# Kernel tuning notes

Hardware: AMD Instinct MI355X
Metric: run time of the kernel (lower is better)

Reference implementation:

```python
import jax, jax.numpy as jnp
import numpy as np

TOP_K = 8
N_GROUP = 8
TOPK_GROUP = 4
ROUTED_SCALING_FACTOR = 2.5
NUM_TOKENS = 131072
NUM_EXPERTS = 256


def setup_inputs() -> dict:
    key = jax.random.key(0)
    k1, k2 = jax.random.split(key)
    logits = jax.random.normal(k1, (NUM_TOKENS, NUM_EXPERTS), dtype=jnp.float32)
    e_score_correction_bias = jax.random.normal(k2, (NUM_EXPERTS,), dtype=jnp.float32)
    return {"logits": logits, "e_score_correction_bias": e_score_correction_bias}


def reference(logits, e_score_correction_bias):
    T, E = logits.shape
    eg = E // N_GROUP  # experts per group
    scores = jax.nn.sigmoid(logits)                       # [T, E]
    swb = scores + e_score_correction_bias                # [T, E]

    # group score = sum of top-2 biased scores within each group
    swb_g = swb.reshape(T, N_GROUP, eg)
    group_scores = jax.lax.top_k(swb_g, 2)[0].sum(-1)     # [T, G]

    # select topk_group groups, build group mask
    group_idx = jax.lax.top_k(group_scores, TOPK_GROUP)[1]  # [T, KG]
    rows = jnp.arange(T)[:, None]
    group_mask = jnp.zeros((T, N_GROUP), dtype=swb.dtype).at[rows, group_idx].set(1.0)
    score_mask = jnp.broadcast_to(group_mask[:, :, None], (T, N_GROUP, eg)).reshape(T, E)

    # mask out non-selected groups, top-k over biased scores
    neg_inf = jnp.array(-jnp.inf, dtype=swb.dtype)
    swb_masked = jnp.where(score_mask > 0, swb, neg_inf)
    topk_idx = jax.lax.top_k(swb_masked, TOP_K)[1]        # [T, K]

    # keep only selected experts' unbiased scores, renormalize, scale
    new_mask = jnp.zeros((T, E), dtype=scores.dtype).at[rows, topk_idx].set(1.0)
    s = scores * new_mask
    s = s / (s.sum(-1, keepdims=True) + 1e-20) * ROUTED_SCALING_FACTOR

    topk_values, topk_indices = jax.lax.top_k(s, TOP_K)   # [T, K]
    return topk_indices.astype(jnp.int32), topk_values.astype(jnp.float32)
```

## Files before the change

### kernel.cpp

```cpp
#include <hip/hip_runtime.h>
#include <cstdint>


constexpr int TOPK_GROUP  = 4;
constexpr int TOP_K       = 8;
constexpr float ROUTED_SCALING = 2.5f;
constexpr unsigned KEY_OFF = 0x3F000000u;

#define DPP_XOR1 0xB1
#define DPP_XOR2 0x4E
#define DPP_HM   0x141
#define DPP_M    0x140

template <int CTRL>
static __device__ __forceinline__ float dpp_f32(float x) {
  return __int_as_float(__builtin_amdgcn_mov_dpp(__float_as_int(x), CTRL, 0xF, 0xF, true));
}
template <int CTRL>
static __device__ __forceinline__ unsigned dpp_u32(unsigned x) {
  return (unsigned)__builtin_amdgcn_mov_dpp((int)x, CTRL, 0xF, 0xF, true);
}

static __device__ __forceinline__ int mbcnt64(unsigned long long m) {
  return __builtin_amdgcn_mbcnt_hi((unsigned)(m >> 32),
         __builtin_amdgcn_mbcnt_lo((unsigned)m, 0));
}

static __device__ __forceinline__ unsigned umax2(unsigned x, unsigned y) {
  return x > y ? x : y;
}

__global__ __launch_bounds__(256) void moe_route_kernel(
    const float* __restrict__ logits,
    const float* __restrict__ bias,
    float* __restrict__ out_idx,
    float* __restrict__ out_val,
    int n_tokens) {
  const int lane = threadIdx.x & 63;
  const int wid  = threadIdx.x >> 6;
  const int token = blockIdx.x * 4 + wid;
  __shared__ float2 buf[4][16];

  const float4 lv = reinterpret_cast<const float4*>(logits)[token * 64 + lane];
  const float4 bv = reinterpret_cast<const float4*>(bias)[lane];

  const float sig0 = __builtin_amdgcn_rcpf(1.0f + __builtin_amdgcn_exp2f(lv.x * -1.44269504f));
  const float sig1 = __builtin_amdgcn_rcpf(1.0f + __builtin_amdgcn_exp2f(lv.y * -1.44269504f));
  const float sig2 = __builtin_amdgcn_rcpf(1.0f + __builtin_amdgcn_exp2f(lv.z * -1.44269504f));
  const float sig3 = __builtin_amdgcn_rcpf(1.0f + __builtin_amdgcn_exp2f(lv.w * -1.44269504f));
  const float swb0 = sig0 + bv.x;
  const float swb1 = sig1 + bv.y;
  const float swb2 = sig2 + bv.z;
  const float swb3 = sig3 + bv.w;

  const float h1 = fmaxf(swb0, swb1), l1 = fminf(swb0, swb1);
  const float h2 = fmaxf(swb2, swb3), l2 = fminf(swb2, swb3);
  float m1 = fmaxf(h1, h2);
  float m2 = fmaxf(fminf(h1, h2), fmaxf(l1, l2));
#define MERGE_LEV(CTRL)                                            \
  {                                                                \
    const float o1 = dpp_f32<CTRL>(m1);                            \
    const float o2 = dpp_f32<CTRL>(m2);                            \
    const float nm1 = fmaxf(m1, o1);                               \
    const float nm2 = fmaxf(fminf(m1, o1), fmaxf(m2, o2));         \
    m1 = nm1; m2 = nm2;                                            \
  }
  MERGE_LEV(DPP_XOR1)
  MERGE_LEV(DPP_XOR2)
  MERGE_LEV(DPP_HM)
#undef MERGE_LEV
  const float gscore = m1 + m2;

  const int g = lane >> 3;
  const int a = lane & 7;
  const float gs_o = __shfl(gscore, a << 3);
  const unsigned long long gm =
      __ballot((gs_o > gscore) || (gs_o == gscore && a < g));
  const int grank = __popc((unsigned)(gm >> (g << 3)) & 0xFFu);
  const bool gsel = grank < TOPK_GROUP;

  const int ebase = lane << 2;
  const unsigned k0 = gsel ? ((unsigned)__float_as_int(fmaxf(swb0, 0.5f)) - KEY_OFF) : 0u;
  const unsigned k1 = gsel ? ((unsigned)__float_as_int(fmaxf(swb1, 0.5f)) - KEY_OFF) : 0u;
  const unsigned k2 = gsel ? ((unsigned)__float_as_int(fmaxf(swb2, 0.5f)) - KEY_OFF) : 0u;
  const unsigned k3 = gsel ? ((unsigned)__float_as_int(fmaxf(swb3, 0.5f)) - KEY_OFF) : 0u;

  unsigned tf = 0u;
  for (int bit = 24; bit >= 16; --bit) {
    const unsigned cand = tf | (1u << bit);
    const int c = __popcll(__ballot(k0 >= cand)) + __popcll(__ballot(k1 >= cand))
                + __popcll(__ballot(k2 >= cand)) + __popcll(__ballot(k3 >= cand));
    if (c >= TOP_K) {
      tf = cand;
      if (c == TOP_K) break;
    }
  }

  bool sel0 = k0 >= tf, sel1 = k1 >= tf, sel2 = k2 >= tf, sel3 = k3 >= tf;
  unsigned long long sm0 = __ballot(sel0), sm1 = __ballot(sel1),
                     sm2 = __ballot(sel2), sm3 = __ballot(sel3);
  const int cnt = __popcll(sm0) + __popcll(sm1) + __popcll(sm2) + __popcll(sm3);

  if (cnt > TOP_K) {
    const unsigned tg = tf + 0x10000u;
    const bool c0 = sel0 && (k0 < tg);
    const bool c1 = sel1 && (k1 < tg);
    const bool c2 = sel2 && (k2 < tg);
    const bool c3 = sel3 && (k3 < tg);
    const int nc = __popcll(__ballot(c0)) + __popcll(__ballot(c1))
                 + __popcll(__ballot(c2)) + __popcll(__ballot(c3));
    const int need2 = TOP_K - (cnt - nc);
    sel0 = sel0 && !c0; sel1 = sel1 && !c1;
    sel2 = sel2 && !c2; sel3 = sel3 && !c3;
    unsigned p0 = c0 ? (((k0 & 0xFFFFu) << 16) | (0xFFFFu - (unsigned)(ebase + 0))) : 0u;
    unsigned p1 = c1 ? (((k1 & 0xFFFFu) << 16) | (0xFFFFu - (unsigned)(ebase + 1))) : 0u;
    unsigned p2 = c2 ? (((k2 & 0xFFFFu) << 16) | (0xFFFFu - (unsigned)(ebase + 2))) : 0u;
    unsigned p3 = c3 ? (((k3 & 0xFFFFu) << 16) | (0xFFFFu - (unsigned)(ebase + 3))) : 0u;
    for (int r = 0; r < need2; ++r) {
      unsigned mm = umax2(umax2(p0, p1), umax2(p2, p3));
      mm = umax2(mm, dpp_u32<DPP_XOR1>(mm));
      mm = umax2(mm, dpp_u32<DPP_XOR2>(mm));
      mm = umax2(mm, dpp_u32<DPP_HM>(mm));
      mm = umax2(mm, dpp_u32<DPP_M>(mm));
      mm = umax2(mm, (unsigned)__shfl_xor((int)mm, 16));
      mm = umax2(mm, (unsigned)__shfl_xor((int)mm, 32));
      const bool w0 = (p0 == mm), w1 = (p1 == mm), w2 = (p2 == mm), w3 = (p3 == mm);
      sel0 = sel0 || w0; sel1 = sel1 || w1;
      sel2 = sel2 || w2; sel3 = sel3 || w3;
      p0 = w0 ? 0u : p0; p1 = w1 ? 0u : p1;
      p2 = w2 ? 0u : p2; p3 = w3 ? 0u : p3;
    }
    sm0 = __ballot(sel0); sm1 = __ballot(sel1);
    sm2 = __ballot(sel2); sm3 = __ballot(sel3);
  }

  const int sbelow = mbcnt64(sm0) + mbcnt64(sm1) + mbcnt64(sm2) + mbcnt64(sm3);
  const int slot0 = sbelow;
  const int slot1 = slot0 + (int)sel0;
  const int slot2 = slot1 + (int)sel1;
  const int slot3 = slot2 + (int)sel2;

  float2* tb = buf[wid];
  tb[sel0 ? slot0 : 8]  = make_float2(__int_as_float(ebase + 0), sig0);
  tb[sel1 ? slot1 : 9]  = make_float2(__int_as_float(ebase + 1), sig1);
  tb[sel2 ? slot2 : 10] = make_float2(__int_as_float(ebase + 2), sig2);
  tb[sel3 ? slot3 : 11] = make_float2(__int_as_float(ebase + 3), sig3);
  asm volatile("s_waitcnt lgkmcnt(0)" ::: "memory");

  const int l8 = lane & 7;
  const float2 w  = tb[l8];
  const float2 wo = tb[lane >> 3];
  const float wsig = w.y;
  float ssum = wsig;
  ssum += dpp_f32<DPP_XOR1>(ssum);
  ssum += dpp_f32<DPP_XOR2>(ssum);
  ssum += dpp_f32<DPP_HM>(ssum);
  const float inv = __builtin_amdgcn_rcpf(ssum);
  const float val = wsig * inv * ROUTED_SCALING;
  const float v_o = wo.y * inv * ROUTED_SCALING;
  const int widx_i = __float_as_int(w.x);
  const int i_o_i  = __float_as_int(wo.x);

  const unsigned long long rm =
      __ballot((val > v_o) || (val == v_o && widx_i < i_o_i));
  const int rank = __popc((unsigned)(rm >> (l8 << 3)) & 0xFFu);

  if (lane < 16) {
    float* base = (lane < 8) ? out_idx : out_val;
    base[token * TOP_K + rank] = (lane < 8) ? (float)widx_i : val;
  }
}

extern "C" void kernel_launch(void* const* d_in, const int* in_sizes, int n_in,
                              void* d_out, int out_size, void* d_ws, size_t ws_size,
                              hipStream_t stream) {
  const float* logits = (const float*)d_in[0];
  const float* bias   = (const float*)d_in[1];
  float* out = (float*)d_out;

  const int n_tokens = in_sizes[0] / 256;
  float* out_idx = out;
  float* out_val = out + (size_t)n_tokens * TOP_K;

  const int blocks = (n_tokens + 3) / 4;
  moe_route_kernel<<<blocks, 256, 0, stream>>>(logits, bias, out_idx, out_val, n_tokens);
}
```

Measured before the change: 41.05 us.

## Process two tokens per wavefront with interleaved selection for ILP

Result: slower. 44.44 us (+8.3%).

```diff
diff --git a/kernel.cpp b/kernel.cpp
--- a/kernel.cpp
+++ b/kernel.cpp
@@ -30,72 +30,15 @@
   return x > y ? x : y;
 }
 
-__global__ __launch_bounds__(256) void moe_route_kernel(
-    const float* __restrict__ logits,
-    const float* __restrict__ bias,
-    float* __restrict__ out_idx,
-    float* __restrict__ out_val,
-    int n_tokens) {
-  const int lane = threadIdx.x & 63;
-  const int wid  = threadIdx.x >> 6;
-  const int token = blockIdx.x * 4 + wid;
-  __shared__ float2 buf[4][16];
-
-  const float4 lv = reinterpret_cast<const float4*>(logits)[token * 64 + lane];
-  const float4 bv = reinterpret_cast<const float4*>(bias)[lane];
-
-  const float sig0 = __builtin_amdgcn_rcpf(1.0f + __builtin_amdgcn_exp2f(lv.x * -1.44269504f));
-  const float sig1 = __builtin_amdgcn_rcpf(1.0f + __builtin_amdgcn_exp2f(lv.y * -1.44269504f));
-  const float sig2 = __builtin_amdgcn_rcpf(1.0f + __builtin_amdgcn_exp2f(lv.z * -1.44269504f));
-  const float sig3 = __builtin_amdgcn_rcpf(1.0f + __builtin_amdgcn_exp2f(lv.w * -1.44269504f));
-  const float swb0 = sig0 + bv.x;
-  const float swb1 = sig1 + bv.y;
-  const float swb2 = sig2 + bv.z;
-  const float swb3 = sig3 + bv.w;
-
-  const float h1 = fmaxf(swb0, swb1), l1 = fminf(swb0, swb1);
-  const float h2 = fmaxf(swb2, swb3), l2 = fminf(swb2, swb3);
-  float m1 = fmaxf(h1, h2);
-  float m2 = fmaxf(fminf(h1, h2), fmaxf(l1, l2));
-#define MERGE_LEV(CTRL)                                            \
-  {                                                                \
-    const float o1 = dpp_f32<CTRL>(m1);                            \
-    const float o2 = dpp_f32<CTRL>(m2);                            \
-    const float nm1 = fmaxf(m1, o1);                               \
-    const float nm2 = fmaxf(fminf(m1, o1), fmaxf(m2, o2));         \
-    m1 = nm1; m2 = nm2;                                            \
-  }
-  MERGE_LEV(DPP_XOR1)
-  MERGE_LEV(DPP_XOR2)
-  MERGE_LEV(DPP_HM)
-#undef MERGE_LEV
-  const float gscore = m1 + m2;
-
-  const int g = lane >> 3;
-  const int a = lane & 7;
-  const float gs_o = __shfl(gscore, a << 3);
-  const unsigned long long gm =
-      __ballot((gs_o > gscore) || (gs_o == gscore && a < g));
-  const int grank = __popc((unsigned)(gm >> (g << 3)) & 0xFFu);
-  const bool gsel = grank < TOPK_GROUP;
-
-  const int ebase = lane << 2;
-  const unsigned k0 = gsel ? ((unsigned)__float_as_int(fmaxf(swb0, 0.5f)) - KEY_OFF) : 0u;
-  const unsigned k1 = gsel ? ((unsigned)__float_as_int(fmaxf(swb1, 0.5f)) - KEY_OFF) : 0u;
-  const unsigned k2 = gsel ? ((unsigned)__float_as_int(fmaxf(swb2, 0.5f)) - KEY_OFF) : 0u;
-  const unsigned k3 = gsel ? ((unsigned)__float_as_int(fmaxf(swb3, 0.5f)) - KEY_OFF) : 0u;
-
-  unsigned tf = 0u;
-  for (int bit = 24; bit >= 16; --bit) {
-    const unsigned cand = tf | (1u << bit);
-    const int c = __popcll(__ballot(k0 >= cand)) + __popcll(__ballot(k1 >= cand))
-                + __popcll(__ballot(k2 >= cand)) + __popcll(__ballot(k3 >= cand));
-    if (c >= TOP_K) {
-      tf = cand;
-      if (c == TOP_K) break;
-    }
-  }
-
+static __device__ __forceinline__ float fast_sig(float x) {
+  return __builtin_amdgcn_rcpf(1.0f + __builtin_amdgcn_exp2f(x * -1.44269504f));
+}
+
+static __device__ __forceinline__ void finish_select(
+    const unsigned k0, const unsigned k1, const unsigned k2, const unsigned k3,
+    const unsigned tf, const int ebase,
+    const float sig0, const float sig1, const float sig2, const float sig3,
+    float2* __restrict__ tb) {
   bool sel0 = k0 >= tf, sel1 = k1 >= tf, sel2 = k2 >= tf, sel3 = k3 >= tf;
   unsigned long long sm0 = __ballot(sel0), sm1 = __ballot(sel1),
                      sm2 = __ballot(sel2), sm3 = __ballot(sel3);
@@ -139,14 +82,15 @@
   const int slot1 = slot0 + (int)sel0;
   const int slot2 = slot1 + (int)sel1;
   const int slot3 = slot2 + (int)sel2;
-
-  float2* tb = buf[wid];
   tb[sel0 ? slot0 : 8]  = make_float2(__int_as_float(ebase + 0), sig0);
   tb[sel1 ? slot1 : 9]  = make_float2(__int_as_float(ebase + 1), sig1);
   tb[sel2 ? slot2 : 10] = make_float2(__int_as_float(ebase + 2), sig2);
   tb[sel3 ? slot3 : 11] = make_float2(__int_as_float(ebase + 3), sig3);
-  asm volatile("s_waitcnt lgkmcnt(0)" ::: "memory");
-
+}
+
+static __device__ __forceinline__ void readback_store(
+    const float2* __restrict__ tb, const int token, const int lane,
+    float* __restrict__ out_idx, float* __restrict__ out_val) {
   const int l8 = lane & 7;
   const float2 w  = tb[l8];
   const float2 wo = tb[lane >> 3];
@@ -160,15 +104,116 @@
   const float v_o = wo.y * inv * ROUTED_SCALING;
   const int widx_i = __float_as_int(w.x);
   const int i_o_i  = __float_as_int(wo.x);
-
   const unsigned long long rm =
       __ballot((val > v_o) || (val == v_o && widx_i < i_o_i));
   const int rank = __popc((unsigned)(rm >> (l8 << 3)) & 0xFFu);
-
   if (lane < 16) {
     float* base = (lane < 8) ? out_idx : out_val;
     base[token * TOP_K + rank] = (lane < 8) ? (float)widx_i : val;
   }
+}
+
+__global__ __launch_bounds__(256) void moe_route_kernel(
+    const float* __restrict__ logits,
+    const float* __restrict__ bias,
+    float* __restrict__ out_idx,
+    float* __restrict__ out_val,
+    int n_tokens) {
+  const int lane = threadIdx.x & 63;
+  const int wid  = threadIdx.x >> 6;
+  const int tA = blockIdx.x * 8 + wid * 2;
+  const int tB = tA + 1;
+  __shared__ float2 buf[4][2][16];
+
+  const float4* lp = reinterpret_cast<const float4*>(logits) + tA * 64 + lane;
+  const float4 lvA = lp[0];
+  const float4 lvB = lp[64];
+  const float4 bv  = reinterpret_cast<const float4*>(bias)[lane];
+
+  const float sigA0 = fast_sig(lvA.x), sigA1 = fast_sig(lvA.y);
+  const float sigA2 = fast_sig(lvA.z), sigA3 = fast_sig(lvA.w);
+  const float sigB0 = fast_sig(lvB.x), sigB1 = fast_sig(lvB.y);
+  const float sigB2 = fast_sig(lvB.z), sigB3 = fast_sig(lvB.w);
+  const float swbA0 = sigA0 + bv.x, swbA1 = sigA1 + bv.y;
+  const float swbA2 = sigA2 + bv.z, swbA3 = sigA3 + bv.w;
+  const float swbB0 = sigB0 + bv.x, swbB1 = sigB1 + bv.y;
+  const float swbB2 = sigB2 + bv.z, swbB3 = sigB3 + bv.w;
+
+  float m1A, m2A, m1B, m2B;
+  {
+    const float h1 = fmaxf(swbA0, swbA1), l1 = fminf(swbA0, swbA1);
+    const float h2 = fmaxf(swbA2, swbA3), l2 = fminf(swbA2, swbA3);
+    m1A = fmaxf(h1, h2);
+    m2A = fmaxf(fminf(h1, h2), fmaxf(l1, l2));
+  }
+  {
+    const float h1 = fmaxf(swbB0, swbB1), l1 = fminf(swbB0, swbB1);
+    const float h2 = fmaxf(swbB2, swbB3), l2 = fminf(swbB2, swbB3);
+    m1B = fmaxf(h1, h2);
+    m2B = fmaxf(fminf(h1, h2), fmaxf(l1, l2));
+  }
+#define MERGE_LEV2(CTRL)                                           \
+  {                                                                \
+    const float oA1 = dpp_f32<CTRL>(m1A);                          \
+    const float oA2 = dpp_f32<CTRL>(m2A);                          \
+    const float oB1 = dpp_f32<CTRL>(m1B);                          \
+    const float oB2 = dpp_f32<CTRL>(m2B);                          \
+    const float nA1 = fmaxf(m1A, oA1);                             \
+    const float nA2 = fmaxf(fminf(m1A, oA1), fmaxf(m2A, oA2));     \
+    const float nB1 = fmaxf(m1B, oB1);                             \
+    const float nB2 = fmaxf(fminf(m1B, oB1), fmaxf(m2B, oB2));     \
+    m1A = nA1; m2A = nA2; m1B = nB1; m2B = nB2;                    \
+  }
+  MERGE_LEV2(DPP_XOR1)
+  MERGE_LEV2(DPP_XOR2)
+  MERGE_LEV2(DPP_HM)
+#undef MERGE_LEV2
+  const float gscoreA = m1A + m2A;
+  const float gscoreB = m1B + m2B;
+
+  const int g = lane >> 3;
+  const int a = lane & 7;
+  const float gsoA = __shfl(gscoreA, a << 3);
+  const float gsoB = __shfl(gscoreB, a << 3);
+  const unsigned long long gmA =
+      __ballot((gsoA > gscoreA) || (gsoA == gscoreA && a < g));
+  const unsigned long long gmB =
+      __ballot((gsoB > gscoreB) || (gsoB == gscoreB && a < g));
+  const bool gselA = __popc((unsigned)(gmA >> (g << 3)) & 0xFFu) < TOPK_GROUP;
+  const bool gselB = __popc((unsigned)(gmB >> (g << 3)) & 0xFFu) < TOPK_GROUP;
+
+  const int ebase = lane << 2;
+  const unsigned kA0 = gselA ? ((unsigned)__float_as_int(fmaxf(swbA0, 0.5f)) - KEY_OFF) : 0u;
+  const unsigned kA1 = gselA ? ((unsigned)__float_as_int(fmaxf(swbA1, 0.5f)) - KEY_OFF) : 0u;
+  const unsigned kA2 = gselA ? ((unsigned)__float_as_int(fmaxf(swbA2, 0.5f)) - KEY_OFF) : 0u;
+  const unsigned kA3 = gselA ? ((unsigned)__float_as_int(fmaxf(swbA3, 0.5f)) - KEY_OFF) : 0u;
+  const unsigned kB0 = gselB ? ((unsigned)__float_as_int(fmaxf(swbB0, 0.5f)) - KEY_OFF) : 0u;
+  const unsigned kB1 = gselB ? ((unsigned)__float_as_int(fmaxf(swbB1, 0.5f)) - KEY_OFF) : 0u;
+  const unsigned kB2 = gselB ? ((unsigned)__float_as_int(fmaxf(swbB2, 0.5f)) - KEY_OFF) : 0u;
+  const unsigned kB3 = gselB ? ((unsigned)__float_as_int(fmaxf(swbB3, 0.5f)) - KEY_OFF) : 0u;
+
+  unsigned tfA = 0u, tfB = 0u;
+  bool doneA = false, doneB = false;
+  for (int bit = 24; bit >= 16; --bit) {
+    const unsigned candA = tfA | (1u << bit);
+    const unsigned candB = tfB | (1u << bit);
+    const int cA = __popcll(__ballot(kA0 >= candA)) + __popcll(__ballot(kA1 >= candA))
+                 + __popcll(__ballot(kA2 >= candA)) + __popcll(__ballot(kA3 >= candA));
+    const int cB = __popcll(__ballot(kB0 >= candB)) + __popcll(__ballot(kB1 >= candB))
+                 + __popcll(__ballot(kB2 >= candB)) + __popcll(__ballot(kB3 >= candB));
+    tfA = (cA >= TOP_K) ? candA : tfA;
+    tfB = (cB >= TOP_K) ? candB : tfB;
+    doneA = doneA || (cA == TOP_K);
+    doneB = doneB || (cB == TOP_K);
+    if (doneA && doneB) break;
+  }
+
+  finish_select(kA0, kA1, kA2, kA3, tfA, ebase, sigA0, sigA1, sigA2, sigA3, buf[wid][0]);
+  finish_select(kB0, kB1, kB2, kB3, tfB, ebase, sigB0, sigB1, sigB2, sigB3, buf[wid][1]);
+  asm volatile("s_waitcnt lgkmcnt(0)" ::: "memory");
+
+  readback_store(buf[wid][0], tA, lane, out_idx, out_val);
+  readback_store(buf[wid][1], tB, lane, out_idx, out_val);
 }
 
 extern "C" void kernel_launch(void* const* d_in, const int* in_sizes, int n_in,
@@ -182,6 +227,6 @@
   float* out_idx = out;
   float* out_val = out + (size_t)n_tokens * TOP_K;
 
-  const int blocks = (n_tokens + 3) / 4;
+  const int blocks = n_tokens / 8;
   moe_route_kernel<<<blocks, 256, 0, stream>>>(logits, bias, out_idx, out_val, n_tokens);
 }
```
